# Performance work log

Measured on AMD Instinct MI355X. Metric: run time of the kernel, lower is better.

## Reference

```python
import jax, jax.numpy as jnp
import numpy as np

K_MASK = -2.3819763e+38
B, T, D = 2, 2048, 2048
N, K, H = 8, 2, 256          # query heads, kv heads, head dim
F = 8192                     # ffn hidden
A = 4                        # num_altup_inputs
P = 4                        # num_modalities
WINDOW = 512
SOFT_CAP = 50.0
Q_SCALE = H ** -0.5
ROPE_BASE = 10000.0


def rms_norm(x, scale=None, eps=1e-6):
    y = x * jax.lax.rsqrt(jnp.mean(jnp.square(x), axis=-1, keepdims=True) + eps)
    if scale is not None:
        y = y * (1.0 + scale)   # scale_plus_one=True
    return y


def apply_rope(x, pos, base=ROPE_BASE, scale_factor=1.0):
    # x: [B,T,num_heads,H], pos: [B,T]
    h = x.shape[-1]
    frac = 2.0 * jnp.arange(h // 2, dtype=jnp.float32) / h
    timescale = base ** frac
    sin_inp = (pos[..., None].astype(jnp.float32) / timescale)[..., None, :] / scale_factor  # [B,T,1,H/2]
    sin, cos = jnp.sin(sin_inp), jnp.cos(sin_inp)
    x1, x2 = jnp.split(x, 2, axis=-1)
    return jnp.concatenate([x1 * cos - x2 * sin, x2 * cos + x1 * sin], axis=-1).astype(x.dtype)


def setup_inputs():
    key = jax.random.key(0)
    ks = jax.random.split(key, 12)
    r = lambda i, shape, s=0.02: jax.random.normal(ks[i], shape, dtype=jnp.float32) * s
    pos = jnp.broadcast_to(jnp.arange(T, dtype=jnp.int32), (B, T))
    causal = pos[:, :, None] >= pos[:, None, :]  # [B,T,T] bool
    return dict(
        x=jax.random.normal(ks[0], (A, B, T, D), dtype=jnp.float32),
        segment_pos=pos,
        attn_mask=causal,
        router_w=r(1, (D, P), 1.0),
        pred_coefs=r(2, (P, A, A), 0.0001),
        corr_coefs=r(3, (P, A), 0.01),
        correct_output_scale=jnp.ones((D,), jnp.float32),
        pre_attn_scale=jnp.zeros((D,), jnp.float32),
        q_w=r(4, (N, D, H)),
        kv_w=r(5, (2, K, D, H)),
        qk_q_scale=jnp.zeros((H,), jnp.float32),
        qk_k_scale=jnp.zeros((H,), jnp.float32),
        o_w=r(6, (N, H, D)),
        post_attn_scale=jnp.zeros((D,), jnp.float32),
        pre_ffw_scale=jnp.zeros((D,), jnp.float32),
        gate_w=r(7, (D, F)),
        up_w=r(8, (D, F)),
        down_w=r(9, (F, D)),
        post_ffw_scale=jnp.zeros((D,), jnp.float32),
    )


def _router(h, router_w):
    # modality router: scale by 1/d_model, project, tanh in fp32
    return jnp.tanh(jnp.einsum('btd,dp->btp', h * (1.0 / D), router_w).astype(jnp.float32))


def _attention(x, segment_pos, attn_mask, q_w, kv_w, qk_q_scale, qk_k_scale, o_w):
    q = jnp.einsum('btd,ndh->btnh', x, q_w)               # [B,T,N,H]
    k, v = jnp.einsum('bsd,ckdh->cbskh', x, kv_w)         # each [B,T,K,H]
    q = rms_norm(q, qk_q_scale)                           # qk norm
    k = rms_norm(k, qk_k_scale)
    v = rms_norm(v)                                       # value norm (no scale)
    q = apply_rope(q, segment_pos) * Q_SCALE
    k = apply_rope(k, segment_pos)
    g = N // K                                            # GQA group size
    qr = q.reshape(B, T, K, g, H)
    logits = jnp.einsum('btkgh,bskh->btkgs', qr, k).reshape(B, T, N, T)
    logits = jnp.tanh(logits / SOFT_CAP) * SOFT_CAP       # attn_logits_soft_cap
    # sliding-window mask combined with causal attn_mask
    sliding = (segment_pos[:, None, :] > segment_pos[:, :, None] - WINDOW) & \
              (segment_pos[:, None, :] < segment_pos[:, :, None] + WINDOW)
    mask = attn_mask & sliding
    padded = jnp.where(mask[:, :, None, :], logits, K_MASK)
    probs = jax.nn.softmax(padded, axis=-1).astype(k.dtype)
    enc = jnp.einsum('btkgs,bskh->btkgh', probs.reshape(B, T, K, g, T), v).reshape(B, T, N, H)
    return jnp.einsum('btnh,nhd->btd', enc, o_w)


def reference(x, segment_pos, attn_mask, router_w, pred_coefs, corr_coefs,
              correct_output_scale, pre_attn_scale, q_w, kv_w, qk_q_scale, qk_k_scale,
              o_w, post_attn_scale, pre_ffw_scale, gate_w, up_w, down_w, post_ffw_scale):
    # ---- AltUp predict ----
    mods = _router(x[0], router_w)                                   # [B,T,P]
    coefs = jnp.einsum('btp,pij->btij', mods, pred_coefs.astype(jnp.float32))
    predictions = x + jnp.einsum('btij,jbtd->ibtd', coefs, x).astype(x.dtype)
    active = predictions[0]
    # ---- attention block ----
    attn_in = rms_norm(active, pre_attn_scale)
    attn = _attention(attn_in, segment_pos, attn_mask, q_w, kv_w, qk_q_scale, qk_k_scale, o_w)
    attn = rms_norm(attn, post_attn_scale)
    attn_gated = active + attn
    # ---- gated-GELU MLP ----
    h = rms_norm(attn_gated, pre_ffw_scale)
    ffw = jnp.einsum('btf,fd->btd', jax.nn.gelu(h @ gate_w) * (h @ up_w), down_w)
    ffw = rms_norm(ffw, post_ffw_scale)
    activated = attn_gated + ffw
    # ---- AltUp correct (with scale_corrected_output) ----
    activated = activated * correct_output_scale
    mods_c = _router(activated, router_w)
    c = jnp.einsum('btp,pi->bti', mods_c, corr_coefs.astype(jnp.float32)) + 1.0
    innovation = activated - predictions[0]
    corrected = predictions + jnp.einsum('bti,btd->ibtd', c, innovation).astype(x.dtype)
    return corrected
```

## Files before the change

### kernel.cpp

```cpp
#include <hip/hip_runtime.h>
#include <hip/hip_bf16.h>

typedef unsigned short u16;
typedef __attribute__((ext_vector_type(8))) short bf16x8_t;
typedef __attribute__((ext_vector_type(4))) float f32x4_t;

#define DEV __device__ __forceinline__

constexpr int cB = 2, cT = 2048, cD = 2048;
constexpr int cN = 8, cK = 2, cH = 256, cF = 8192;
constexpr int cBT = cB * cT;
constexpr float cEPS = 1e-6f;
constexpr float cQS = 0.0625f;
constexpr float cCAP = 50.0f;
constexpr int cWIN = 512;
constexpr int cNH = 12;

DEV u16 f2bf(float f) {
  union { float f; unsigned u; } c; c.f = f;
  unsigned u = c.u;
  return (u16)((u + 0x7fffu + ((u >> 16) & 1u)) >> 16);
}
DEV float bf2f(u16 h) {
  union { unsigned u; float f; } c; c.u = ((unsigned)h) << 16;
  return c.f;
}
DEV float g4(const float4& v, int k) { return k == 0 ? v.x : k == 1 ? v.y : k == 2 ? v.z : v.w; }
DEV void store_bf4(u16* p, float a, float b, float c, float d) {
  union { u16 h[4]; uint2 v; } o;
  o.h[0] = f2bf(a); o.h[1] = f2bf(b); o.h[2] = f2bf(c); o.h[3] = f2bf(d);
  *(uint2*)p = o.v;
}
DEV float tanh_fast(float x) {
  float e2 = __expf(2.0f * x);
  return 1.0f - 2.0f * __builtin_amdgcn_rcpf(e2 + 1.0f);
}
DEV float gelu_fast(float x) {
  float u = 1.5957691216057308f * (x + 0.044715f * x * x * x);
  float e2 = __expf(u);
  return x * (1.0f - __builtin_amdgcn_rcpf(e2 + 1.0f));
}

DEV float block_sum256(float v, float* sbuf) {
  #pragma unroll
  for (int m = 32; m > 0; m >>= 1) v += __shfl_xor(v, m, 64);
  int wid = threadIdx.x >> 6;
  if ((threadIdx.x & 63) == 0) sbuf[wid] = v;
  __syncthreads();
  float tot = sbuf[0] + sbuf[1] + sbuf[2] + sbuf[3];
  __syncthreads();
  return tot;
}
DEV void block_sum256x4(float v[4], float* sbuf ) {
  #pragma unroll
  for (int m = 32; m > 0; m >>= 1) {
    #pragma unroll
    for (int k = 0; k < 4; k++) v[k] += __shfl_xor(v[k], m, 64);
  }
  int wid = threadIdx.x >> 6;
  if ((threadIdx.x & 63) == 0) *(float4*)(sbuf + wid * 4) = make_float4(v[0], v[1], v[2], v[3]);
  __syncthreads();
  #pragma unroll
  for (int k = 0; k < 4; k++) v[k] = sbuf[k] + sbuf[4 + k] + sbuf[8 + k] + sbuf[12 + k];
  __syncthreads();
}

#define GLD_LDS16(gp, lp) __builtin_amdgcn_global_load_lds( \
    (const __attribute__((address_space(1))) void*)(gp),    \
    (__attribute__((address_space(3))) void*)(lp), 16, 0, 0)

#define WAITV(n) asm volatile("s_waitcnt vmcnt(" #n ")" ::: "memory")

__global__ __launch_bounds__(256) void k_transpose_cast(
    const float* __restrict__ src, u16* __restrict__ dst, int R, int C, int gu) {
  __shared__ float tile[32][33];
  size_t base = (size_t)blockIdx.z * R * C;
  int c0 = blockIdx.x * 32, r0 = blockIdx.y * 32;
  int tx = threadIdx.x & 31, ty = threadIdx.x >> 5;
  #pragma unroll
  for (int i = 0; i < 4; i++)
    tile[ty + i * 8][tx] = src[base + (size_t)(r0 + ty + i * 8) * C + c0 + tx];
  __syncthreads();
  #pragma unroll
  for (int i = 0; i < 4; i++) {
    int c = c0 + ty + i * 8;
    int n = (gu < 0) ? c : (((c >> 4) << 5) + (gu << 4) + (c & 15));
    dst[base + (size_t)n * R + r0 + tx] = f2bf(tile[tx][ty + i * 8]);
  }
}

__global__ __launch_bounds__(256) void k_rope_table(
    const int* __restrict__ pos, float2* __restrict__ rt) {
  int idx = blockIdx.x * 256 + threadIdx.x;
  int bt = idx >> 7, j = idx & 127;
  float p = (float)pos[bt];
  float ts = powf(10000.0f, (2.0f * j) * (1.0f / cH));
  float si = p / ts;
  rt[idx] = make_float2(sinf(si), cosf(si));
}

__global__ __launch_bounds__(256) void k_predict(
    const float* __restrict__ x, const float* __restrict__ router_w,
    const float* __restrict__ pred_coefs, const float* __restrict__ pre_attn_scale,
    float* __restrict__ out, u16* __restrict__ attn_in) {
  __shared__ float sbuf[16];
  int bt = blockIdx.x, tid = threadIdx.x;
  const size_t PL = (size_t)cBT * cD;
  const size_t rowb = (size_t)bt * cD;
  float4 xv[4][2];
  #pragma unroll
  for (int j = 0; j < 4; j++)
    #pragma unroll
    for (int u = 0; u < 2; u++)
      xv[j][u] = *(const float4*)(x + j * PL + rowb + (u * 256 + tid) * 4);
  float rp[4] = {0, 0, 0, 0};
  #pragma unroll
  for (int u = 0; u < 2; u++)
    #pragma unroll
    for (int k = 0; k < 4; k++) {
      int e = (u * 256 + tid) * 4 + k;
      float4 rw = *(const float4*)(router_w + (size_t)e * 4);
      float xe = g4(xv[0][u], k);
      rp[0] += xe * rw.x; rp[1] += xe * rw.y; rp[2] += xe * rw.z; rp[3] += xe * rw.w;
    }
  block_sum256x4(rp, sbuf);
  float mods[4];
  #pragma unroll
  for (int p = 0; p < 4; p++) mods[p] = tanh_fast(rp[p] * (1.0f / cD));
  float coef[4][4];
  #pragma unroll
  for (int i = 0; i < 4; i++)
    #pragma unroll
    for (int j = 0; j < 4; j++) {
      float s = 0;
      #pragma unroll
      for (int p = 0; p < 4; p++) s += mods[p] * pred_coefs[(p * 4 + i) * 4 + j];
      coef[i][j] = s;
    }
  float4 p04[2]; float ssq = 0;
  #pragma unroll
  for (int u = 0; u < 2; u++)
    #pragma unroll
    for (int i = 0; i < 4; i++) {
      float4 s = xv[i][u];
      #pragma unroll
      for (int j = 0; j < 4; j++) {
        s.x += coef[i][j] * xv[j][u].x; s.y += coef[i][j] * xv[j][u].y;
        s.z += coef[i][j] * xv[j][u].z; s.w += coef[i][j] * xv[j][u].w;
      }
      *(float4*)(out + i * PL + rowb + (u * 256 + tid) * 4) = s;
      if (i == 0) { p04[u] = s; ssq += s.x * s.x + s.y * s.y + s.z * s.z + s.w * s.w; }
    }
  float rs = rsqrtf(block_sum256(ssq, sbuf) * (1.0f / cD) + cEPS);
  #pragma unroll
  for (int u = 0; u < 2; u++) {
    int e0 = (u * 256 + tid) * 4;
    float4 sc = *(const float4*)(pre_attn_scale + e0);
    store_bf4(attn_in + rowb + e0,
              p04[u].x * rs * (1.0f + sc.x), p04[u].y * rs * (1.0f + sc.y),
              p04[u].z * rs * (1.0f + sc.z), p04[u].w * rs * (1.0f + sc.w));
  }
}

template <int OUT_MODE>
__global__ __launch_bounds__(512, 2) void k_gemm8w(
    const u16* __restrict__ A, const u16* __restrict__ Bt, void* __restrict__ Cv,
    int Nn, int Kk) {
  constexpr int MI = 8;
  constexpr int BM = MI * 32;
  constexpr int A_KS = BM * 32;
  constexpr int B_KS = 256 * 32;
  constexpr int BUF_E = 2 * A_KS + 2 * B_KS;
  extern __shared__ u16 lds[];

  const int tid = threadIdx.x;
  const int wid = tid >> 6, lane = tid & 63;
  const int wr = wid >> 2, wc = wid & 3;
  const int fr = lane & 15, fq = lane >> 4;

  const int nwg = gridDim.x * gridDim.y;
  const int flat = blockIdx.y * gridDim.x + blockIdx.x;
  const int swz = (flat & 7) * (nwg >> 3) + (flat >> 3);
  const int m0 = (swz % gridDim.x) * BM;
  const int n0 = (swz / gridDim.x) * 256;
  const int NT = Kk >> 6;

  const int srow = lane >> 2, sslot = lane & 3;

  auto stageA = [&](int t, int ks) {
    u16* buf = lds + (t & 1) * BUF_E + ks * A_KS;
    #pragma unroll
    for (int i = 0; i < BM / 128; i++) {
      int row0 = i * 128 + wid * 16;
      int row = row0 + srow;
      int col = (sslot ^ ((row >> 1) & 3)) * 8;
      GLD_LDS16(A + (size_t)(m0 + row) * Kk + t * 64 + ks * 32 + col, buf + row0 * 32);
    }
  };
  auto stageB = [&](int t, int ks) {
    u16* buf = lds + (t & 1) * BUF_E + 2 * A_KS + ks * B_KS;
    #pragma unroll
    for (int i = 0; i < 2; i++) {
      int row0 = i * 128 + wid * 16;
      int row = row0 + srow;
      int col = (sslot ^ ((row >> 1) & 3)) * 8;
      GLD_LDS16(Bt + (size_t)(n0 + row) * Kk + t * 64 + ks * 32 + col, buf + row0 * 32);
    }
  };
  auto readA = [&](const u16* buf, int ks, int i) -> bf16x8_t {
    int row = wr * (MI * 16) + i * 16 + fr;
    return *(const bf16x8_t*)(buf + ks * A_KS + row * 32 + (fq ^ ((row >> 1) & 3)) * 8);
  };
  auto readB = [&](const u16* buf, int ks, int j) -> bf16x8_t {
    int row = wc * 64 + j * 16 + fr;
    return *(const bf16x8_t*)(buf + 2 * A_KS + ks * B_KS + row * 32 + (fq ^ ((row >> 1) & 3)) * 8);
  };

  f32x4_t acc[MI][4];
  #pragma unroll
  for (int i = 0; i < MI; i++)
    #pragma unroll
    for (int j = 0; j < 4; j++) acc[i][j] = (f32x4_t){0.f, 0.f, 0.f, 0.f};

  stageA(0, 0); stageB(0, 0); stageA(0, 1); stageB(0, 1);
  WAITV(4);
  __builtin_amdgcn_s_barrier();

#define PHASE_MFMA(J0)                                                              \
  __builtin_amdgcn_s_setprio(1);                                                    \
  _Pragma("unroll")                                                                 \
  for (int i = 0; i < MI; i++) {                                                    \
    acc[i][J0]     = __builtin_amdgcn_mfma_f32_16x16x32_bf16(a0[i], b0[0], acc[i][J0], 0, 0, 0);     \
    acc[i][J0 + 1] = __builtin_amdgcn_mfma_f32_16x16x32_bf16(a0[i], b0[1], acc[i][J0 + 1], 0, 0, 0); \
  }                                                                                 \
  __builtin_amdgcn_s_setprio(0);

  for (int t = 0; t < NT; t++) {
    const u16* buf = lds + (t & 1) * BUF_E;
    const bool pf = (t + 1 < NT);
    bf16x8_t a0[MI], b0[2];

    #pragma unroll
    for (int i = 0; i < MI; i++) a0[i] = readA(buf, 0, i);
    b0[0] = readB(buf, 0, 0); b0[1] = readB(buf, 0, 1);
    if (pf) stageA(t + 1, 0);
    __builtin_amdgcn_s_barrier();
    PHASE_MFMA(0)
    __builtin_amdgcn_s_barrier();

    b0[0] = readB(buf, 0, 2); b0[1] = readB(buf, 0, 3);
    if (pf) stageB(t + 1, 0);
    if (pf) WAITV(4); else WAITV(0);
    __builtin_amdgcn_s_barrier();
    PHASE_MFMA(2)
    __builtin_amdgcn_s_barrier();

    #pragma unroll
    for (int i = 0; i < MI; i++) a0[i] = readA(buf, 1, i);
    b0[0] = readB(buf, 1, 0); b0[1] = readB(buf, 1, 1);
    if (pf) stageA(t + 1, 1);
    __builtin_amdgcn_s_barrier();
    PHASE_MFMA(0)
    __builtin_amdgcn_s_barrier();

    b0[0] = readB(buf, 1, 2); b0[1] = readB(buf, 1, 3);
    if (pf) stageB(t + 1, 1);
    if (pf) WAITV(4);
    __builtin_amdgcn_s_barrier();
    PHASE_MFMA(2)
    __builtin_amdgcn_s_barrier();
  }
#undef PHASE_MFMA

  if constexpr (OUT_MODE == 2) {
    const int Nh = Nn >> 1;
    #pragma unroll
    for (int i = 0; i < MI; i++)
      #pragma unroll
      for (int jp = 0; jp < 2; jp++) {
        int c = (n0 + wc * 64 + jp * 32) / 2 + fr;
        #pragma unroll
        for (int r = 0; r < 4; r++) {
          int m = m0 + wr * (MI * 16) + i * 16 + fq * 4 + r;
          float g = acc[i][2 * jp][r], uu = acc[i][2 * jp + 1][r];
          ((u16*)Cv)[(size_t)m * Nh + c] = f2bf(gelu_fast(g) * uu);
        }
      }
  } else {
    #pragma unroll
    for (int i = 0; i < MI; i++)
      #pragma unroll
      for (int j = 0; j < 4; j++)
        #pragma unroll
        for (int r = 0; r < 4; r++) {
          int m = m0 + wr * (MI * 16) + i * 16 + fq * 4 + r;
          int n = n0 + wc * 64 + j * 16 + fr;
          ((u16*)Cv)[(size_t)m * Nn + n] = f2bf(acc[i][j][r]);
        }
  }
}

template <int OUT_MODE>
__global__ __launch_bounds__(512, 2) void k_gemm4r(
    const u16* __restrict__ A, const u16* __restrict__ Bt, void* __restrict__ Cv,
    int Nn, int Kk) {
  constexpr int MI = 4;
  constexpr int BM = 128;
  constexpr int A_KS = BM * 32;
  constexpr int B_KS = 256 * 32;
  constexpr int SLOT_E = 2 * A_KS + 2 * B_KS;
  extern __shared__ u16 lds[];

  const int tid = threadIdx.x;
  const int wid = tid >> 6, lane = tid & 63;
  const int wr = wid >> 2, wc = wid & 3;
  const int fr = lane & 15, fq = lane >> 4;

  const int nwg = gridDim.x * gridDim.y;
  const int flat = blockIdx.y * gridDim.x + blockIdx.x;
  const int swz = (flat & 7) * (nwg >> 3) + (flat >> 3);
  const int m0 = (swz % gridDim.x) * BM;
  const int n0 = (swz / gridDim.x) * 256;
  const int NT = Kk >> 6;

  const int srow = lane >> 2, sslot = lane & 3;

  auto stageA = [&](int t, int ks) {
    u16* buf = lds + (t % 3) * SLOT_E + ks * A_KS;
    int row0 = wid * 16;
    int row = row0 + srow;
    int col = (sslot ^ ((row >> 1) & 3)) * 8;
    GLD_LDS16(A + (size_t)(m0 + row) * Kk + t * 64 + ks * 32 + col, buf + row0 * 32);
  };
  auto stageB = [&](int t, int ks) {
    u16* buf = lds + (t % 3) * SLOT_E + 2 * A_KS + ks * B_KS;
    #pragma unroll
    for (int i = 0; i < 2; i++) {
      int row0 = i * 128 + wid * 16;
      int row = row0 + srow;
      int col = (sslot ^ ((row >> 1) & 3)) * 8;
      GLD_LDS16(Bt + (size_t)(n0 + row) * Kk + t * 64 + ks * 32 + col, buf + row0 * 32);
    }
  };
  auto readA = [&](const u16* buf, int ks, int i) -> bf16x8_t {
    int row = wr * 64 + i * 16 + fr;
    return *(const bf16x8_t*)(buf + ks * A_KS + row * 32 + (fq ^ ((row >> 1) & 3)) * 8);
  };
  auto readB = [&](const u16* buf, int ks, int j) -> bf16x8_t {
    int row = wc * 64 + j * 16 + fr;
    return *(const bf16x8_t*)(buf + 2 * A_KS + ks * B_KS + row * 32 + (fq ^ ((row >> 1) & 3)) * 8);
  };

  f32x4_t acc[MI][4];
  #pragma unroll
  for (int i = 0; i < MI; i++)
    #pragma unroll
    for (int j = 0; j < 4; j++) acc[i][j] = (f32x4_t){0.f, 0.f, 0.f, 0.f};

  stageA(0, 0); stageB(0, 0); stageA(0, 1); stageB(0, 1);
  stageA(1, 0); stageB(1, 0); stageA(1, 1); stageB(1, 1);
  WAITV(9);
  __builtin_amdgcn_s_barrier();

#define PHASE_MFMA4(J0)                                                             \
  __builtin_amdgcn_s_setprio(1);                                                    \
  _Pragma("unroll")                                                                 \
  for (int i = 0; i < MI; i++) {                                                    \
    acc[i][J0]     = __builtin_amdgcn_mfma_f32_16x16x32_bf16(a0[i], b0[0], acc[i][J0], 0, 0, 0);     \
    acc[i][J0 + 1] = __builtin_amdgcn_mfma_f32_16x16x32_bf16(a0[i], b0[1], acc[i][J0 + 1], 0, 0, 0); \
  }                                                                                 \
  __builtin_amdgcn_s_setprio(0);

  for (int t = 0; t < NT; t++) {
    const u16* buf = lds + (t % 3) * SLOT_E;
    const bool pf2 = (t + 2 < NT);
    const bool pf1 = (t + 1 < NT);
    bf16x8_t a0[MI], b0[2];

    #pragma unroll
    for (int i = 0; i < MI; i++) a0[i] = readA(buf, 0, i);
    b0[0] = readB(buf, 0, 0); b0[1] = readB(buf, 0, 1);
    if (pf2) stageA(t + 2, 0);
    __builtin_amdgcn_s_barrier();
    PHASE_MFMA4(0)
    __builtin_amdgcn_s_barrier();

    b0[0] = readB(buf, 0, 2); b0[1] = readB(buf, 0, 3);
    if (pf2) stageB(t + 2, 0);
    if (pf2) WAITV(9); else if (pf1) WAITV(6); else WAITV(0);
    __builtin_amdgcn_s_barrier();
    PHASE_MFMA4(2)
    __builtin_amdgcn_s_barrier();

    #pragma unroll
    for (int i = 0; i < MI; i++) a0[i] = readA(buf, 1, i);
    b0[0] = readB(buf, 1, 0); b0[1] = readB(buf, 1, 1);
    if (pf2) stageA(t + 2, 1);
    __builtin_amdgcn_s_barrier();
    PHASE_MFMA4(0)
    __builtin_amdgcn_s_barrier();

    b0[0] = readB(buf, 1, 2); b0[1] = readB(buf, 1, 3);
    if (pf2) stageB(t + 2, 1);
    if (pf2) WAITV(9); else if (pf1) WAITV(3);
    __builtin_amdgcn_s_barrier();
    PHASE_MFMA4(2)
    __builtin_amdgcn_s_barrier();
  }
#undef PHASE_MFMA4

  #pragma unroll
  for (int i = 0; i < MI; i++)
    #pragma unroll
    for (int j = 0; j < 4; j++)
      #pragma unroll
      for (int r = 0; r < 4; r++) {
        int m = m0 + wr * 64 + i * 16 + fq * 4 + r;
        int n = n0 + wc * 64 + j * 16 + fr;
        float v = acc[i][j][r];
        if (OUT_MODE == 1) ((u16*)Cv)[(size_t)m * Nn + n] = f2bf(v);
        else ((float*)Cv)[(size_t)m * Nn + n] = v;
      }
}

__global__ __launch_bounds__(64) void k_qkvpost(
    u16* __restrict__ qkv, const float* __restrict__ qscale,
    const float* __restrict__ kscale, const float2* __restrict__ rt,
    u16* __restrict__ vT) {
  int h = blockIdx.x % cNH, bt = blockIdx.x / cNH;
  int lane = threadIdx.x;
  u16* row = qkv + ((size_t)bt * cNH + h) * cH;
  float v[4], ssq = 0;
  #pragma unroll
  for (int m = 0; m < 4; m++) { v[m] = bf2f(row[lane + 64 * m]); ssq += v[m] * v[m]; }
  #pragma unroll
  for (int mm = 32; mm > 0; mm >>= 1) ssq += __shfl_xor(ssq, mm, 64);
  float rs = rsqrtf(ssq * (1.0f / cH) + cEPS);
  if (h < 10) {
    const float* sc = (h < 8) ? qscale : kscale;
    float os = (h < 8) ? cQS : 1.0f;
    #pragma unroll
    for (int m = 0; m < 4; m++) {
      int e = lane + 64 * m;
      v[m] = v[m] * rs * (1.0f + sc[e]);
    }
    #pragma unroll
    for (int m = 0; m < 2; m++) {
      int j = lane + 64 * m;
      float2 t = rt[bt * 128 + j];
      float x1 = v[m], x2 = v[m + 2];
      row[j]       = f2bf((x1 * t.y - x2 * t.x) * os);
      row[j + 128] = f2bf((x2 * t.y + x1 * t.x) * os);
    }
  } else {
    int kk = h - 10;
    int b = bt / cT, t = bt % cT;
    #pragma unroll
    for (int m = 0; m < 4; m++) {
      int e = lane + 64 * m;
      vT[((size_t)(b * cK + kk) * cH + e) * cT + t] = f2bf(v[m] * rs);
    }
  }
}

__global__ __launch_bounds__(64) void k_attn(
    const u16* __restrict__ qkv, const u16* __restrict__ vT, u16* __restrict__ enc) {
  int t0 = blockIdx.x * 16;
  int n = blockIdx.y, b = blockIdx.z;
  int kn = n >> 2;
  int lane = threadIdx.x;
  int fr = lane & 15, fq = lane >> 4;
  __shared__ float P[16][33];

  bf16x8_t qf[8];
  const u16* qrow = qkv + ((size_t)(b * cT + t0 + fr) * cNH + n) * cH;
  #pragma unroll
  for (int ks = 0; ks < 8; ks++) qf[ks] = *(const bf16x8_t*)(qrow + ks * 32 + fq * 8);

  f32x4_t acc[16];
  #pragma unroll
  for (int ht = 0; ht < 16; ht++) acc[ht] = (f32x4_t){0.f, 0.f, 0.f, 0.f};
  float psum[4] = {0.f, 0.f, 0.f, 0.f};

  int s_lo = t0 - (cWIN - 1); if (s_lo < 0) s_lo = 0; s_lo &= ~31;
  for (int s0 = s_lo; s0 <= t0 + 15; s0 += 32) {
    f32x4_t S[2];
    S[0] = (f32x4_t){0.f, 0.f, 0.f, 0.f};
    S[1] = (f32x4_t){0.f, 0.f, 0.f, 0.f};
    #pragma unroll
    for (int c = 0; c < 2; c++) {
      const u16* krow = qkv + ((size_t)(b * cT + s0 + c * 16 + fr) * cNH + 8 + kn) * cH;
      #pragma unroll
      for (int ks = 0; ks < 8; ks++) {
        bf16x8_t kf = *(const bf16x8_t*)(krow + ks * 32 + fq * 8);
        S[c] = __builtin_amdgcn_mfma_f32_16x16x32_bf16(qf[ks], kf, S[c], 0, 0, 0);
      }
    }
    #pragma unroll
    for (int c = 0; c < 2; c++) {
      int s = s0 + c * 16 + fr;
      #pragma unroll
      for (int r = 0; r < 4; r++) {
        int t = t0 + fq * 4 + r;
        float l = cCAP * tanh_fast(S[c][r] * (1.0f / cCAP));
        float pe = (s <= t && s >= t - (cWIN - 1)) ? __expf(l) : 0.0f;
        psum[r] += pe;
        P[fq * 4 + r][c * 16 + fr] = pe;
      }
    }
    bf16x8_t pf;
    #pragma unroll
    for (int e = 0; e < 8; e++) pf[e] = (short)f2bf(P[fr][fq * 8 + e]);
    #pragma unroll
    for (int ht = 0; ht < 16; ht++) {
      bf16x8_t vf = *(const bf16x8_t*)(vT + (((size_t)(b * cK + kn)) * cH + ht * 16 + fr) * cT + s0 + fq * 8);
      acc[ht] = __builtin_amdgcn_mfma_f32_16x16x32_bf16(pf, vf, acc[ht], 0, 0, 0);
    }
  }
  #pragma unroll
  for (int r = 0; r < 4; r++) {
    #pragma unroll
    for (int m = 1; m < 16; m <<= 1) psum[r] += __shfl_xor(psum[r], m, 64);
  }
  float inv[4];
  #pragma unroll
  for (int r = 0; r < 4; r++) inv[r] = 1.0f / psum[r];
  #pragma unroll
  for (int ht = 0; ht < 16; ht++)
    #pragma unroll
    for (int r = 0; r < 4; r++)
      enc[(((size_t)(b * cT + t0 + fq * 4 + r)) * cN + n) * cH + ht * 16 + fr] =
          f2bf(acc[ht][r] * inv[r]);
}

__global__ __launch_bounds__(256) void k_postattn(
    const float* __restrict__ attn_raw, const float* __restrict__ out0,
    const float* __restrict__ post_attn_scale, const float* __restrict__ pre_ffw_scale,
    float* __restrict__ ag, u16* __restrict__ h) {
  __shared__ float sbuf[4];
  int bt = blockIdx.x, tid = threadIdx.x;
  const size_t rowb = (size_t)bt * cD;
  float4 ar[2]; float ssq = 0;
  #pragma unroll
  for (int u = 0; u < 2; u++) {
    ar[u] = *(const float4*)(attn_raw + rowb + (u * 256 + tid) * 4);
    ssq += ar[u].x * ar[u].x + ar[u].y * ar[u].y + ar[u].z * ar[u].z + ar[u].w * ar[u].w;
  }
  float rs = rsqrtf(block_sum256(ssq, sbuf) * (1.0f / cD) + cEPS);
  float4 agv[2]; float ssq2 = 0;
  #pragma unroll
  for (int u = 0; u < 2; u++) {
    int e0 = (u * 256 + tid) * 4;
    float4 o0 = *(const float4*)(out0 + rowb + e0);
    float4 sc = *(const float4*)(post_attn_scale + e0);
    float4 a;
    a.x = o0.x + ar[u].x * rs * (1.0f + sc.x);
    a.y = o0.y + ar[u].y * rs * (1.0f + sc.y);
    a.z = o0.z + ar[u].z * rs * (1.0f + sc.z);
    a.w = o0.w + ar[u].w * rs * (1.0f + sc.w);
    agv[u] = a;
    *(float4*)(ag + rowb + e0) = a;
    ssq2 += a.x * a.x + a.y * a.y + a.z * a.z + a.w * a.w;
  }
  float rs2 = rsqrtf(block_sum256(ssq2, sbuf) * (1.0f / cD) + cEPS);
  #pragma unroll
  for (int u = 0; u < 2; u++) {
    int e0 = (u * 256 + tid) * 4;
    float4 sc = *(const float4*)(pre_ffw_scale + e0);
    store_bf4(h + rowb + e0,
              agv[u].x * rs2 * (1.0f + sc.x), agv[u].y * rs2 * (1.0f + sc.y),
              agv[u].z * rs2 * (1.0f + sc.z), agv[u].w * rs2 * (1.0f + sc.w));
  }
}

__global__ __launch_bounds__(256) void k_final(
    const float* __restrict__ ffw_raw, const float* __restrict__ ag,
    const float* __restrict__ post_ffw_scale, const float* __restrict__ cos_scale,
    const float* __restrict__ router_w, const float* __restrict__ corr_coefs,
    float* __restrict__ out) {
  __shared__ float sbuf[16];
  int bt = blockIdx.x, tid = threadIdx.x;
  const size_t PL = (size_t)cBT * cD;
  const size_t rowb = (size_t)bt * cD;
  float4 fv[2]; float ssq = 0;
  #pragma unroll
  for (int u = 0; u < 2; u++) {
    fv[u] = *(const float4*)(ffw_raw + rowb + (u * 256 + tid) * 4);
    ssq += fv[u].x * fv[u].x + fv[u].y * fv[u].y + fv[u].z * fv[u].z + fv[u].w * fv[u].w;
  }
  float rs = rsqrtf(block_sum256(ssq, sbuf) * (1.0f / cD) + cEPS);
  float4 av[2];
  float rp[4] = {0, 0, 0, 0};
  #pragma unroll
  for (int u = 0; u < 2; u++) {
    int e0 = (u * 256 + tid) * 4;
    float4 agx = *(const float4*)(ag + rowb + e0);
    float4 ps = *(const float4*)(post_ffw_scale + e0);
    float4 cs = *(const float4*)(cos_scale + e0);
    float4 a;
    a.x = (agx.x + fv[u].x * rs * (1.0f + ps.x)) * cs.x;
    a.y = (agx.y + fv[u].y * rs * (1.0f + ps.y)) * cs.y;
    a.z = (agx.z + fv[u].z * rs * (1.0f + ps.z)) * cs.z;
    a.w = (agx.w + fv[u].w * rs * (1.0f + ps.w)) * cs.w;
    av[u] = a;
    #pragma unroll
    for (int k = 0; k < 4; k++) {
      float4 rw = *(const float4*)(router_w + (size_t)(e0 + k) * 4);
      float xe = g4(a, k);
      rp[0] += xe * rw.x; rp[1] += xe * rw.y; rp[2] += xe * rw.z; rp[3] += xe * rw.w;
    }
  }
  block_sum256x4(rp, sbuf);
  float cc[4];
  #pragma unroll
  for (int i = 0; i < 4; i++) {
    float s = 1.0f;
    #pragma unroll
    for (int p = 0; p < 4; p++) s += tanh_fast(rp[p] * (1.0f / cD)) * corr_coefs[p * 4 + i];
    cc[i] = s;
  }
  #pragma unroll
  for (int u = 0; u < 2; u++) {
    size_t o = rowb + (u * 256 + tid) * 4;
    float4 p0 = *(const float4*)(out + o);
    float4 in4;
    in4.x = av[u].x - p0.x; in4.y = av[u].y - p0.y;
    in4.z = av[u].z - p0.z; in4.w = av[u].w - p0.w;
    float4 w0;
    w0.x = p0.x + cc[0] * in4.x; w0.y = p0.y + cc[0] * in4.y;
    w0.z = p0.z + cc[0] * in4.z; w0.w = p0.w + cc[0] * in4.w;
    *(float4*)(out + o) = w0;
    #pragma unroll
    for (int i = 1; i < 4; i++) {
      float4 q = *(const float4*)(out + i * PL + o);
      q.x += cc[i] * in4.x; q.y += cc[i] * in4.y;
      q.z += cc[i] * in4.z; q.w += cc[i] * in4.w;
      *(float4*)(out + i * PL + o) = q;
    }
  }
}

extern "C" void kernel_launch(void* const* d_in, const int* in_sizes, int n_in,
                              void* d_out, int out_size, void* d_ws, size_t ws_size,
                              hipStream_t stream) {
  const float* x              = (const float*)d_in[0];
  const int*   pos            = (const int*)d_in[1];
  const float* router_w       = (const float*)d_in[3];
  const float* pred_coefs     = (const float*)d_in[4];
  const float* corr_coefs     = (const float*)d_in[5];
  const float* cos_scale      = (const float*)d_in[6];
  const float* pre_attn_scale = (const float*)d_in[7];
  const float* q_w            = (const float*)d_in[8];
  const float* kv_w           = (const float*)d_in[9];
  const float* qk_q_scale     = (const float*)d_in[10];
  const float* qk_k_scale     = (const float*)d_in[11];
  const float* o_w            = (const float*)d_in[12];
  const float* post_attn_scale= (const float*)d_in[13];
  const float* pre_ffw_scale  = (const float*)d_in[14];
  const float* gate_w         = (const float*)d_in[15];
  const float* up_w           = (const float*)d_in[16];
  const float* down_w         = (const float*)d_in[17];
  const float* post_ffw_scale = (const float*)d_in[18];
  float* out = (float*)d_out;

  char* wsp = (char*)d_ws;
  size_t off = 0;
  auto take = [&](size_t nbytes) -> char* {
    char* p = wsp + off;
    off += (nbytes + 255) & ~((size_t)255);
    return p;
  };
  u16* gu_wT    = (u16*)take((size_t)2 * cF * cD * 2);
  u16* down_wT  = (u16*)take((size_t)cD * cF * 2);
  u16* qkv_wT   = (u16*)take((size_t)cNH * cH * cD * 2);
  u16* o_wT     = (u16*)take((size_t)cD * cN * cH * 2);
  u16* attn_in  = (u16*)take((size_t)cBT * cD * 2);
  u16* qkvbuf   = (u16*)take((size_t)cBT * cNH * cH * 2);
  u16* vTbuf    = (u16*)take((size_t)cB * cK * cH * cT * 2);
  u16* encbuf   = (u16*)take((size_t)cBT * cN * cH * 2);
  float* attn_raw = (float*)take((size_t)cBT * cD * 4);
  float* agbuf    = (float*)take((size_t)cBT * cD * 4);
  u16* hbuf     = (u16*)take((size_t)cBT * cD * 2);
  u16* Gcbuf    = (u16*)take((size_t)cBT * cF * 2);
  float* ffw_raw = (float*)take((size_t)cBT * cD * 4);
  float2* ropetab = (float2*)take((size_t)cBT * 128 * 8);
  (void)in_sizes; (void)n_in; (void)out_size; (void)ws_size;

  dim3 blk256(256), blk64(64), blk512(512);
  constexpr unsigned LDS8  = 2 * (2 * 256 * 32 + 2 * 256 * 32) * 2;
  constexpr unsigned LDS4R = 3 * (2 * 128 * 32 + 2 * 256 * 32) * 2;

  k_transpose_cast<<<dim3(cF / 32, cD / 32, 1), blk256, 0, stream>>>(gate_w, gu_wT, cD, cF, 0);
  k_transpose_cast<<<dim3(cF / 32, cD / 32, 1), blk256, 0, stream>>>(up_w, gu_wT, cD, cF, 1);
  k_transpose_cast<<<dim3(cD / 32, cF / 32, 1), blk256, 0, stream>>>(down_w, down_wT, cF, cD, -1);
  k_transpose_cast<<<dim3(cH / 32, cD / 32, cN), blk256, 0, stream>>>(q_w, qkv_wT, cD, cH, -1);
  k_transpose_cast<<<dim3(cH / 32, cD / 32, 2 * cK), blk256, 0, stream>>>(
      kv_w, qkv_wT + (size_t)cN * cH * cD, cD, cH, -1);
  k_transpose_cast<<<dim3(cD / 32, (cN * cH) / 32, 1), blk256, 0, stream>>>(o_w, o_wT, cN * cH, cD, -1);
  k_rope_table<<<dim3(cBT * 128 / 256), blk256, 0, stream>>>(pos, ropetab);

  k_predict<<<dim3(cBT), blk256, 0, stream>>>(x, router_w, pred_coefs, pre_attn_scale, out, attn_in);

  k_gemm4r<1><<<dim3(cBT / 128, (cNH * cH) / 256), blk512, LDS4R, stream>>>(
      attn_in, qkv_wT, qkvbuf, cNH * cH, cD);

  k_qkvpost<<<dim3(cBT * cNH), blk64, 0, stream>>>(qkvbuf, qk_q_scale, qk_k_scale, ropetab, vTbuf);

  k_attn<<<dim3(cT / 16, cN, cB), blk64, 0, stream>>>(qkvbuf, vTbuf, encbuf);

  k_gemm4r<0><<<dim3(cBT / 128, cD / 256), blk512, LDS4R, stream>>>(
      encbuf, o_wT, attn_raw, cD, cN * cH);
  k_postattn<<<dim3(cBT), blk256, 0, stream>>>(attn_raw, out, post_attn_scale, pre_ffw_scale, agbuf, hbuf);

  k_gemm8w<2><<<dim3(cBT / 256, (2 * cF) / 256), blk512, LDS8, stream>>>(
      hbuf, gu_wT, Gcbuf, 2 * cF, cD);
  k_gemm4r<0><<<dim3(cBT / 128, cD / 256), blk512, LDS4R, stream>>>(
      Gcbuf, down_wT, ffw_raw, cD, cF);

  k_final<<<dim3(cBT), blk256, 0, stream>>>(ffw_raw, agbuf, post_ffw_scale, cos_scale,
                                            router_w, corr_coefs, out);
}
```

Before: 961.8 us.

## Vectorize weight transpose-cast with 64x64 tiles and deepen gemm8w prefetch

The weight transpose/cast kernel now uses 64x64 tiles with float4 global loads and 4-wide bf16 stores, cutting per-element memory instructions when converting the fp32 weights. Separately, the 8-wave GEMM main loop is restaged to prefetch half-tiles further ahead (t+1 second half and t+2 first half) with deeper vmcnt waits, so global-to-LDS loads get more time to land before use. The deeper prefetch reuses the same two LDS buffers and its correctness depends on the barrier/wait ordering. The larger tile raises LDS use per block in the transpose kernel.

```diff
diff --git a/kernel.cpp b/kernel.cpp
--- a/kernel.cpp
+++ b/kernel.cpp
@@ -73,19 +73,26 @@
 
 __global__ __launch_bounds__(256) void k_transpose_cast(
     const float* __restrict__ src, u16* __restrict__ dst, int R, int C, int gu) {
-  __shared__ float tile[32][33];
+  __shared__ float tile[64][65];
   size_t base = (size_t)blockIdx.z * R * C;
-  int c0 = blockIdx.x * 32, r0 = blockIdx.y * 32;
-  int tx = threadIdx.x & 31, ty = threadIdx.x >> 5;
-  #pragma unroll
-  for (int i = 0; i < 4; i++)
-    tile[ty + i * 8][tx] = src[base + (size_t)(r0 + ty + i * 8) * C + c0 + tx];
+  int c0 = blockIdx.x * 64, r0 = blockIdx.y * 64;
+  int tx = threadIdx.x & 15, ty = threadIdx.x >> 4;
+  #pragma unroll
+  for (int i = 0; i < 4; i++) {
+    int r = ty + i * 16;
+    float4 v = *(const float4*)(src + base + (size_t)(r0 + r) * C + c0 + tx * 4);
+    tile[r][tx * 4 + 0] = v.x; tile[r][tx * 4 + 1] = v.y;
+    tile[r][tx * 4 + 2] = v.z; tile[r][tx * 4 + 3] = v.w;
+  }
   __syncthreads();
   #pragma unroll
   for (int i = 0; i < 4; i++) {
-    int c = c0 + ty + i * 8;
+    int j = ty + i * 16;
+    int c = c0 + j;
     int n = (gu < 0) ? c : (((c >> 4) << 5) + (gu << 4) + (c & 15));
-    dst[base + (size_t)n * R + r0 + tx] = f2bf(tile[tx][ty + i * 8]);
+    store_bf4(dst + base + (size_t)n * R + r0 + tx * 4,
+              tile[tx * 4 + 0][j], tile[tx * 4 + 1][j],
+              tile[tx * 4 + 2][j], tile[tx * 4 + 3][j]);
   }
 }
 
@@ -223,7 +230,8 @@
     for (int j = 0; j < 4; j++) acc[i][j] = (f32x4_t){0.f, 0.f, 0.f, 0.f};
 
   stageA(0, 0); stageB(0, 0); stageA(0, 1); stageB(0, 1);
-  WAITV(4);
+  stageA(1, 0); stageB(1, 0);
+  WAITV(8);
   __builtin_amdgcn_s_barrier();
 
 #define PHASE_MFMA(J0)                                                              \
@@ -237,20 +245,21 @@
 
   for (int t = 0; t < NT; t++) {
     const u16* buf = lds + (t & 1) * BUF_E;
-    const bool pf = (t + 1 < NT);
+    const bool p1 = (t + 1 < NT);
+    const bool p2 = (t + 2 < NT);
     bf16x8_t a0[MI], b0[2];
 
     #pragma unroll
     for (int i = 0; i < MI; i++) a0[i] = readA(buf, 0, i);
     b0[0] = readB(buf, 0, 0); b0[1] = readB(buf, 0, 1);
-    if (pf) stageA(t + 1, 0);
+    if (p1) stageA(t + 1, 1);
     __builtin_amdgcn_s_barrier();
     PHASE_MFMA(0)
     __builtin_amdgcn_s_barrier();
 
     b0[0] = readB(buf, 0, 2); b0[1] = readB(buf, 0, 3);
-    if (pf) stageB(t + 1, 0);
-    if (pf) WAITV(4); else WAITV(0);
+    if (p1) stageB(t + 1, 1);
+    if (p1) WAITV(8); else WAITV(0);
     __builtin_amdgcn_s_barrier();
     PHASE_MFMA(2)
     __builtin_amdgcn_s_barrier();
@@ -258,14 +267,14 @@
     #pragma unroll
     for (int i = 0; i < MI; i++) a0[i] = readA(buf, 1, i);
     b0[0] = readB(buf, 1, 0); b0[1] = readB(buf, 1, 1);
-    if (pf) stageA(t + 1, 1);
+    if (p2) stageA(t + 2, 0);
     __builtin_amdgcn_s_barrier();
     PHASE_MFMA(0)
     __builtin_amdgcn_s_barrier();
 
     b0[0] = readB(buf, 1, 2); b0[1] = readB(buf, 1, 3);
-    if (pf) stageB(t + 1, 1);
-    if (pf) WAITV(4);
+    if (p2) stageB(t + 2, 0);
+    if (p2) WAITV(8); else if (p1) WAITV(4);
     __builtin_amdgcn_s_barrier();
     PHASE_MFMA(2)
     __builtin_amdgcn_s_barrier();
@@ -690,13 +699,13 @@
   constexpr unsigned LDS8  = 2 * (2 * 256 * 32 + 2 * 256 * 32) * 2;
   constexpr unsigned LDS4R = 3 * (2 * 128 * 32 + 2 * 256 * 32) * 2;
 
-  k_transpose_cast<<<dim3(cF / 32, cD / 32, 1), blk256, 0, stream>>>(gate_w, gu_wT, cD, cF, 0);
-  k_transpose_cast<<<dim3(cF / 32, cD / 32, 1), blk256, 0, stream>>>(up_w, gu_wT, cD, cF, 1);
-  k_transpose_cast<<<dim3(cD / 32, cF / 32, 1), blk256, 0, stream>>>(down_w, down_wT, cF, cD, -1);
-  k_transpose_cast<<<dim3(cH / 32, cD / 32, cN), blk256, 0, stream>>>(q_w, qkv_wT, cD, cH, -1);
-  k_transpose_cast<<<dim3(cH / 32, cD / 32, 2 * cK), blk256, 0, stream>>>(
+  k_transpose_cast<<<dim3(cF / 64, cD / 64, 1), blk256, 0, stream>>>(gate_w, gu_wT, cD, cF, 0);
+  k_transpose_cast<<<dim3(cF / 64, cD / 64, 1), blk256, 0, stream>>>(up_w, gu_wT, cD, cF, 1);
+  k_transpose_cast<<<dim3(cD / 64, cF / 64, 1), blk256, 0, stream>>>(down_w, down_wT, cF, cD, -1);
+  k_transpose_cast<<<dim3(cH / 64, cD / 64, cN), blk256, 0, stream>>>(q_w, qkv_wT, cD, cH, -1);
+  k_transpose_cast<<<dim3(cH / 64, cD / 64, 2 * cK), blk256, 0, stream>>>(
       kv_w, qkv_wT + (size_t)cN * cH * cD, cD, cH, -1);
-  k_transpose_cast<<<dim3(cD / 32, (cN * cH) / 32, 1), blk256, 0, stream>>>(o_w, o_wT, cN * cH, cD, -1);
+  k_transpose_cast<<<dim3(cD / 64, (cN * cH) / 64, 1), blk256, 0, stream>>>(o_w, o_wT, cN * cH, cD, -1);
   k_rope_table<<<dim3(cBT * 128 / 256), blk256, 0, stream>>>(pos, ropetab);
 
   k_predict<<<dim3(cBT), blk256, 0, stream>>>(x, router_w, pred_coefs, pre_attn_scale, out, attn_in);
```

Result: no change. 950.6 us (-1.2%).
